# Performance work log

Hardware: AMD Instinct MI355X
Metric: run time of the kernel (lower is better)

Reference implementation:

```python
import jax, jax.numpy as jnp
import numpy as np

C = 512
C8 = C // 8  # query/key projection dim


def _conv1x1(x, W, b):
    # x: [B,C,H,W], W: [O,C], b: [O] -> [B,O,H,W]
    return jnp.einsum('bchw,oc->bohw', x, W) + b[None, :, None, None]


def setup_inputs() -> dict:
    key = jax.random.key(0)
    ks = jax.random.split(key, 13)
    B, H, Wd = 4, 64, 64
    s = 0.02
    return {
        'x_rgb': jax.random.normal(ks[0], (B, C, H, Wd), jnp.float32),
        'x_dep': jax.random.normal(ks[1], (B, C, H, Wd), jnp.float32),
        'Wq': jax.random.normal(ks[2], (C8, C), jnp.float32) * s,
        'bq': jnp.zeros((C8,), jnp.float32),
        'Wk': jax.random.normal(ks[3], (C8, C), jnp.float32) * s,
        'bk': jnp.zeros((C8,), jnp.float32),
        'Wdq': jax.random.normal(ks[4], (C8, C), jnp.float32) * s,
        'bdq': jnp.zeros((C8,), jnp.float32),
        'Wdk': jax.random.normal(ks[5], (C8, C), jnp.float32) * s,
        'bdk': jnp.zeros((C8,), jnp.float32),
        'Wv': jax.random.normal(ks[6], (C, C), jnp.float32) * s,
        'bv': jnp.zeros((C,), jnp.float32),
        'gamma': jnp.zeros((1,), jnp.float32),
    }


def reference(x_rgb, x_dep, Wq, bq, Wk, bk, Wdq, bdq, Wdk, bdk, Wv, bv, gamma):
    B, Cc, H, Wd = x_rgb.shape
    N = H * Wd
    # 1x1 conv projections, flattened over spatial positions -> [B, c, N]
    q = _conv1x1(x_rgb, Wq, bq).reshape(B, C8, N)
    k = _conv1x1(x_rgb, Wk, bk).reshape(B, C8, N)
    qd = _conv1x1(x_dep, Wdq, bdq).reshape(B, C8, N)
    kd = _conv1x1(x_dep, Wdk, bdk).reshape(B, C8, N)
    # fused dual-stream energy: [B, N, N]
    energy = jnp.einsum('bci,bcj->bij', q, k) + jnp.einsum('bci,bcj->bij', qd, kd)
    attention = jax.nn.softmax(energy, axis=-1)
    v = _conv1x1(x_rgb, Wv, bv).reshape(B, Cc, N)
    # out[b,c,i] = sum_j v[b,c,j] * attention[b,i,j]
    out = jnp.einsum('bcj,bij->bci', v, attention).reshape(B, Cc, H, Wd)
    return gamma[0] * out + x_rgb
```

## Files before the change

### kernel.cpp

```cpp
#include <hip/hip_runtime.h>
#include <math.h>

#define B_ 4
#define C_ 512
#define D_ 128
#define N_ 4096

typedef short s4v __attribute__((ext_vector_type(4)));
typedef short s8v __attribute__((ext_vector_type(8)));
typedef float f4v __attribute__((ext_vector_type(4)));

__device__ __forceinline__ unsigned short f2bf(float x) {
    union { float f; unsigned u; } v; v.f = x;
    unsigned r = v.u + 0x7FFF + ((v.u >> 16) & 1);
    return (unsigned short)(r >> 16);
}
__device__ __forceinline__ float bf2f(unsigned short h) {
    union { unsigned u; float f; } v; v.u = ((unsigned)h) << 16; return v.f;
}

__global__ __launch_bounds__(256) void cvt_w_kernel(
    const float* __restrict__ Wq,  const float* __restrict__ bq,
    const float* __restrict__ Wk,  const float* __restrict__ bk,
    const float* __restrict__ Wdq, const float* __restrict__ bdq,
    const float* __restrict__ Wdk, const float* __restrict__ bdk,
    const float* __restrict__ Wv,  const float* __restrict__ bv,
    unsigned short* __restrict__ Wb, float* __restrict__ biasb)
{
    int t = blockIdx.x * 256 + threadIdx.x;
    int e0 = t * 8;
    int row = e0 >> 9, c = e0 & 511;
    const float* src; int r0;
    if (row < 64)       { src = Wq;  r0 = row; }
    else if (row < 128) { src = Wk;  r0 = row - 64; }
    else if (row < 640) { src = Wv;  r0 = row - 128; }
    else if (row < 704) { src = Wdq; r0 = row - 640; }
    else                { src = Wdk; r0 = row - 704; }
    const float* p = src + (size_t)r0 * 512 + c;
    s8v o;
    #pragma unroll
    for (int u = 0; u < 8; ++u) ((unsigned short*)&o)[u] = f2bf(p[u]);
    *(s8v*)&Wb[e0] = o;
    if (blockIdx.x == 0) {
        #pragma unroll
        for (int s = 0; s < 3; ++s) {
            int o2 = threadIdx.x + 256 * s;
            float v;
            if (o2 < 64)       v = bq[o2];
            else if (o2 < 128) v = bk[o2 - 64];
            else if (o2 < 640) v = bv[o2 - 128];
            else if (o2 < 704) v = bdq[o2 - 640];
            else               v = bdk[o2 - 704];
            biasb[o2] = v;
        }
    }
}

__global__ __launch_bounds__(256) void xpose_kernel(
    const float* __restrict__ x_rgb, const float* __restrict__ x_dep,
    unsigned short* __restrict__ Xt)
{
    __shared__ __align__(16) unsigned short Ls[64 * 72];
    const int cT = blockIdx.x & 7, iT = blockIdx.x >> 3;
    const int b = blockIdx.y, st = blockIdx.z;
    const int t = threadIdx.x;
    const float* Xb = (st ? x_dep : x_rgb) + (size_t)b * C_ * N_;

    const int c4 = t >> 4, i4 = t & 15;
    {
        const float* xp = Xb + (size_t)(cT * 64 + c4 * 4) * N_ + iT * 64 + i4 * 4;
        float4 r0 = *(const float4*)(xp);
        float4 r1 = *(const float4*)(xp + N_);
        float4 r2 = *(const float4*)(xp + 2 * N_);
        float4 r3 = *(const float4*)(xp + 3 * N_);
        s4v p0 = { (short)f2bf(r0.x), (short)f2bf(r1.x), (short)f2bf(r2.x), (short)f2bf(r3.x) };
        s4v p1 = { (short)f2bf(r0.y), (short)f2bf(r1.y), (short)f2bf(r2.y), (short)f2bf(r3.y) };
        s4v p2 = { (short)f2bf(r0.z), (short)f2bf(r1.z), (short)f2bf(r2.z), (short)f2bf(r3.z) };
        s4v p3 = { (short)f2bf(r0.w), (short)f2bf(r1.w), (short)f2bf(r2.w), (short)f2bf(r3.w) };
        *(s4v*)&Ls[(i4 * 4 + 0) * 72 + c4 * 4] = p0;
        *(s4v*)&Ls[(i4 * 4 + 1) * 72 + c4 * 4] = p1;
        *(s4v*)&Ls[(i4 * 4 + 2) * 72 + c4 * 4] = p2;
        *(s4v*)&Ls[(i4 * 4 + 3) * 72 + c4 * 4] = p3;
    }
    __syncthreads();
    unsigned short* dst = Xt + ((size_t)(st * 4 + b) * N_ + iT * 64) * 512 + cT * 64;
    #pragma unroll
    for (int s = 0; s < 2; ++s) {
        int lin = t + 256 * s;
        int row = lin >> 3, g = lin & 7;
        *(s8v*)&dst[(size_t)row * 512 + g * 8] = *(const s8v*)&Ls[row * 72 + g * 8];
    }
}

__global__ __launch_bounds__(256) void gemm_kernel(
    const unsigned short* __restrict__ Wb, const float* __restrict__ biasb,
    const unsigned short* __restrict__ Xt,
    unsigned short* __restrict__ Q, unsigned short* __restrict__ K,
    unsigned short* __restrict__ V)
{
    __shared__ __align__(16) unsigned short Ws[128 * 64];
    __shared__ __align__(16) unsigned short Xs[128 * 64];
    const int b  = blockIdx.x >> 5;
    const int i0 = (blockIdx.x & 31) * 128;
    const int by = blockIdx.y;
    const int mbase = by * 128;
    const int st = (by == 5);
    const int t = threadIdx.x, w = t >> 6;
    const int lane = t & 63, col = lane & 15, quad = lane >> 4;
    const int mh = (w & 1) * 64, nh = (w >> 1) * 64;

    const unsigned short* Wg = Wb + (size_t)mbase * 512;
    const unsigned short* Xg = Xt + ((size_t)(st * 4 + b) * N_ + i0) * 512;

    f4v acc[4][4];
    #pragma unroll
    for (int mt = 0; mt < 4; ++mt)
        #pragma unroll
        for (int nt = 0; nt < 4; ++nt) acc[mt][nt] = (f4v){0.f, 0.f, 0.f, 0.f};

    for (int kc = 0; kc < 8; ++kc) {
        const int k0 = kc * 64;
        s8v wt[4], xt[4];
        #pragma unroll
        for (int s = 0; s < 4; ++s) {
            int lin = t + 256 * s;
            int row = lin >> 3, g = lin & 7;
            wt[s] = *(const s8v*)&Wg[(size_t)row * 512 + k0 + g * 8];
            xt[s] = *(const s8v*)&Xg[(size_t)row * 512 + k0 + g * 8];
        }
        __syncthreads();
        #pragma unroll
        for (int s = 0; s < 4; ++s) {
            int lin = t + 256 * s;
            int row = lin >> 3, g = lin & 7;
            int soff = row * 64 + ((g ^ (row & 7)) * 8);
            *(s8v*)&Ws[soff] = wt[s];
            *(s8v*)&Xs[soff] = xt[s];
        }
        __syncthreads();
        #pragma unroll
        for (int kk = 0; kk < 2; ++kk) {
            const int gq = kk * 4 + quad;
            s8v af[4], bf[4];
            #pragma unroll
            for (int mt = 0; mt < 4; ++mt) {
                int r = mh + mt * 16 + col;
                af[mt] = *(const s8v*)&Ws[r * 64 + ((gq ^ (r & 7)) * 8)];
            }
            #pragma unroll
            for (int nt = 0; nt < 4; ++nt) {
                int r = nh + nt * 16 + col;
                bf[nt] = *(const s8v*)&Xs[r * 64 + ((gq ^ (r & 7)) * 8)];
            }
            #pragma unroll
            for (int nt = 0; nt < 4; ++nt)
                #pragma unroll
                for (int mt = 0; mt < 4; ++mt)
                    acc[mt][nt] = __builtin_amdgcn_mfma_f32_16x16x32_bf16(
                        af[mt], bf[nt], acc[mt][nt], 0, 0, 0);
        }
    }

    const int mlo0 = mbase + mh;
    #pragma unroll
    for (int mt = 0; mt < 4; ++mt) {
        const int mlo = mlo0 + mt * 16;
        f4v bi = *(const f4v*)&biasb[mlo + quad * 4];
        if (mlo < 128 || mlo >= 640) {
            unsigned short* dst; int dbase;
            if (mlo < 64)       { dst = Q; dbase = mlo; }
            else if (mlo < 128) { dst = K; dbase = mlo - 64; }
            else if (mlo < 704) { dst = Q; dbase = 64 + (mlo - 640); }
            else                { dst = K; dbase = 64 + (mlo - 704); }
            #pragma unroll
            for (int nt = 0; nt < 4; ++nt) {
                int i = i0 + nh + nt * 16 + col;
                s4v pk = { (short)f2bf(acc[mt][nt][0] + bi[0]),
                           (short)f2bf(acc[mt][nt][1] + bi[1]),
                           (short)f2bf(acc[mt][nt][2] + bi[2]),
                           (short)f2bf(acc[mt][nt][3] + bi[3]) };
                *(s4v*)&dst[((size_t)b * N_ + i) * D_ + dbase + quad * 4] = pk;
            }
        } else {
            int c0 = mlo - 128 + quad * 4;
            #pragma unroll
            for (int nt = 0; nt < 4; ++nt) {
                int i = i0 + nh + nt * 16 + col;
                #pragma unroll
                for (int r = 0; r < 4; ++r)
                    V[((size_t)b * C_ + c0 + r) * N_ + i] =
                        f2bf(acc[mt][nt][r] + bi[r]);
            }
        }
    }
}

__global__ __launch_bounds__(256, 2) void attn_kernel(
    const unsigned short* __restrict__ Q, const unsigned short* __restrict__ K,
    const unsigned short* __restrict__ V,
    unsigned short* __restrict__ O_ws, float* __restrict__ l_ws)
{
    __shared__ __align__(16) unsigned short Ks[2][32 * 136];
    __shared__ __align__(16) unsigned short Ps[2][64 * 40];
    __shared__ float lred[2][64];

    const int id  = blockIdx.x;
    const int grp = id & 7;
    const int b   = grp & 3;
    const int jh  = grp >> 2;
    const int it  = id >> 3;
    const int i0  = it * 64;
    const int jb  = jh * 2048;
    const int t = threadIdx.x, w = t >> 6;
    const int lane = t & 63, col = lane & 15, quad = lane >> 4;
    const int ih = w & 1, jq = w >> 1;

    const unsigned short* Kg = K + (size_t)b * N_ * D_;
    const unsigned short* Vg = V + (size_t)b * C_ * N_;

    s8v qf[2][4];
    #pragma unroll
    for (int ig = 0; ig < 2; ++ig) {
        const unsigned short* qr =
            Q + ((size_t)b * N_ + i0 + ih * 32 + ig * 16 + col) * D_ + quad * 8;
        #pragma unroll
        for (int kk = 0; kk < 4; ++kk) qf[ig][kk] = *(const s8v*)(qr + kk * 32);
    }

    f4v accO[4][8];
    #pragma unroll
    for (int rt = 0; rt < 4; ++rt)
        #pragma unroll
        for (int ct = 0; ct < 8; ++ct) accO[rt][ct] = (f4v){0.f, 0.f, 0.f, 0.f};
    float lsum[2] = {0.f, 0.f};

    const unsigned short* Vt = Vg + (size_t)(w * 128 + col) * N_ + quad * 8;

    #pragma unroll
    for (int s = 0; s < 2; ++s) {
        int gi = t + 256 * s;
        s8v kv = *(const s8v*)&Kg[(size_t)(jb + (gi >> 4)) * D_ + (gi & 15) * 8];
        *(s8v*)&Ks[0][(gi >> 4) * 136 + (gi & 15) * 8] = kv;
    }
    asm volatile("s_waitcnt lgkmcnt(0)" ::: "memory");
    __builtin_amdgcn_s_barrier();

    for (int tt = 0; tt < 64; ++tt) {
        const int cur = tt & 1;
        const int j0 = jb + tt * 32;

        s8v kt[2];
        if (tt < 63) {
            #pragma unroll
            for (int s = 0; s < 2; ++s) {
                int gi = t + 256 * s;
                kt[s] = *(const s8v*)&Kg[(size_t)(j0 + 32 + (gi >> 4)) * D_ + (gi & 15) * 8];
            }
        }
        __builtin_amdgcn_sched_barrier(0);
        s8v vf[8];
        #pragma unroll
        for (int ct = 0; ct < 8; ++ct)
            vf[ct] = *(const s8v*)(Vt + (size_t)(ct * 16) * N_ + j0);

        f4v s0 = (f4v){0.f, 0.f, 0.f, 0.f};
        f4v s1 = (f4v){0.f, 0.f, 0.f, 0.f};
        #pragma unroll
        for (int kk = 0; kk < 4; ++kk) {
            s8v kf = *(const s8v*)&Ks[cur][(jq * 16 + col) * 136 + kk * 32 + quad * 8];
            s0 = __builtin_amdgcn_mfma_f32_16x16x32_bf16(kf, qf[0][kk], s0, 0, 0, 0);
            s1 = __builtin_amdgcn_mfma_f32_16x16x32_bf16(kf, qf[1][kk], s1, 0, 0, 0);
        }
        #pragma unroll
        for (int ig = 0; ig < 2; ++ig) {
            f4v sv = ig ? s1 : s0;
            s4v p; float ls = 0.f;
            #pragma unroll
            for (int r = 0; r < 4; ++r) {
                float e = __expf(sv[r]);
                ls += e;
                p[r] = (short)f2bf(e);
            }
            lsum[ig] += ls;
            *(s4v*)&Ps[cur][(ih * 32 + ig * 16 + col) * 40 + jq * 16 + quad * 4] = p;
        }
        if (tt < 63) {
            #pragma unroll
            for (int s = 0; s < 2; ++s) {
                int gi = t + 256 * s;
                *(s8v*)&Ks[cur ^ 1][(gi >> 4) * 136 + (gi & 15) * 8] = kt[s];
            }
        }
        asm volatile("s_waitcnt lgkmcnt(0)" ::: "memory");
        __builtin_amdgcn_s_barrier();

        s8v pf[4];
        #pragma unroll
        for (int rt = 0; rt < 4; ++rt)
            pf[rt] = *(const s8v*)&Ps[cur][(rt * 16 + col) * 40 + quad * 8];
        __builtin_amdgcn_s_setprio(1);
        #pragma unroll
        for (int ct = 0; ct < 8; ++ct)
            #pragma unroll
            for (int rt = 0; rt < 4; ++rt)
                accO[rt][ct] = __builtin_amdgcn_mfma_f32_16x16x32_bf16(
                    pf[rt], vf[ct], accO[rt][ct], 0, 0, 0);
        __builtin_amdgcn_s_setprio(0);
    }

    #pragma unroll
    for (int ig = 0; ig < 2; ++ig) {
        float v = lsum[ig];
        v += __shfl_xor(v, 16);
        v += __shfl_xor(v, 32);
        if (quad == 0) lred[jq][ih * 32 + ig * 16 + col] = v;
    }
    __syncthreads();
    if (t < 64)
        l_ws[((size_t)jh * B_ + b) * N_ + i0 + t] = lred[0][t] + lred[1][t];

    const size_t wbase =
        ((((size_t)jh * B_ + b) * 64 + it) * 4 + w) * 8192;
    #pragma unroll
    for (int ct = 0; ct < 8; ++ct)
        #pragma unroll
        for (int rt = 0; rt < 4; ++rt) {
            s4v pk = { (short)f2bf(accO[rt][ct][0]), (short)f2bf(accO[rt][ct][1]),
                       (short)f2bf(accO[rt][ct][2]), (short)f2bf(accO[rt][ct][3]) };
            *(s4v*)&O_ws[wbase + (size_t)(ct * 4 + rt) * 256 + lane * 4] = pk;
        }
}

__global__ __launch_bounds__(256) void combine_kernel(
    const unsigned short* __restrict__ O_ws, const float* __restrict__ l_ws,
    const float* __restrict__ x_rgb, const float* __restrict__ gamma,
    float* __restrict__ out)
{
    const size_t half = (size_t)B_ * 64 * 4 * 8192;
    int idx = blockIdx.x * 256 + threadIdx.x;
    int i4 = idx & 1023;
    int c  = (idx >> 10) & 511;
    int b  = idx >> 19;
    int i  = i4 * 4;
    int i0b = i >> 6, il = i & 63;
    int rt = il >> 4, qd = (il >> 2) & 3;
    int w = c >> 7, cl = c & 127, ct = cl >> 4, col = cl & 15;
    size_t obase = (((size_t)b * 64 + i0b) * 4 + w) * 8192
                 + (size_t)(ct * 4 + rt) * 256 + (qd * 16 + col) * 4;
    s4v o0 = *(const s4v*)&O_ws[obase];
    s4v o1 = *(const s4v*)&O_ws[half + obase];
    float4 l0 = *(const float4*)&l_ws[(size_t)b * N_ + i];
    float4 l1 = *(const float4*)&l_ws[(size_t)(B_ + b) * N_ + i];
    size_t base = ((size_t)b * C_ + c) * N_ + i;
    float4 x4 = *(const float4*)&x_rgb[base];
    float g = gamma[0];
    float4 r;
    r.x = g * (bf2f((unsigned short)o0[0]) + bf2f((unsigned short)o1[0])) / (l0.x + l1.x) + x4.x;
    r.y = g * (bf2f((unsigned short)o0[1]) + bf2f((unsigned short)o1[1])) / (l0.y + l1.y) + x4.y;
    r.z = g * (bf2f((unsigned short)o0[2]) + bf2f((unsigned short)o1[2])) / (l0.z + l1.z) + x4.z;
    r.w = g * (bf2f((unsigned short)o0[3]) + bf2f((unsigned short)o1[3])) / (l0.w + l1.w) + x4.w;
    *(float4*)&out[base] = r;
}

extern "C" void kernel_launch(void* const* d_in, const int* in_sizes, int n_in,
                              void* d_out, int out_size, void* d_ws, size_t ws_size,
                              hipStream_t stream) {
    (void)in_sizes; (void)n_in; (void)out_size; (void)ws_size;
    const float* x_rgb = (const float*)d_in[0];
    const float* x_dep = (const float*)d_in[1];
    const float* Wq    = (const float*)d_in[2];
    const float* bq    = (const float*)d_in[3];
    const float* Wk    = (const float*)d_in[4];
    const float* bk    = (const float*)d_in[5];
    const float* Wdq   = (const float*)d_in[6];
    const float* bdq   = (const float*)d_in[7];
    const float* Wdk   = (const float*)d_in[8];
    const float* bdk   = (const float*)d_in[9];
    const float* Wv    = (const float*)d_in[10];
    const float* bv    = (const float*)d_in[11];
    const float* gamma = (const float*)d_in[12];
    float* out = (float*)d_out;

    unsigned short* Q     = (unsigned short*)d_ws;
    unsigned short* K     = Q + (size_t)B_ * N_ * D_;
    unsigned short* V     = K + (size_t)B_ * N_ * D_;
    unsigned short* Wb    = V + (size_t)B_ * C_ * N_;
    float*          biasb = (float*)(Wb + 768 * 512);
    unsigned short* XtO   = (unsigned short*)(biasb + 1024);
    float*          l_ws  = (float*)(XtO + (size_t)2 * B_ * C_ * N_);

    cvt_w_kernel<<<dim3(192), 256, 0, stream>>>(
        Wq, bq, Wk, bk, Wdq, bdq, Wdk, bdk, Wv, bv, Wb, biasb);
    xpose_kernel<<<dim3(512, 4, 2), 256, 0, stream>>>(x_rgb, x_dep, XtO);
    gemm_kernel<<<dim3(128, 6), 256, 0, stream>>>(Wb, biasb, XtO, Q, K, V);
    attn_kernel<<<dim3(512), 256, 0, stream>>>(Q, K, V, XtO, l_ws);
    combine_kernel<<<dim3(8192), 256, 0, stream>>>(XtO, l_ws, x_rgb, gamma, out);
}
```

Measured before the change: 308.6 us.

## Stage V tiles through swizzled LDS with register prefetch instead of direct global loads

Each V tile (512 channels x 32 positions) is now loaded cooperatively with coalesced 16-byte reads into registers one iteration ahead, then written to a swizzled shared-memory buffer. The PV MFMA operands are read from LDS rather than through per-wave strided global loads. P is single-buffered and a second barrier per iteration is added, and the QK MFMAs get raised priority. The intent is to improve V load coalescing and hide its latency, at the cost of extra LDS traffic (32 KB more shared memory, which may reduce occupancy), more registers and an extra barrier.

```diff
diff --git a/kernel.cpp b/kernel.cpp
--- a/kernel.cpp
+++ b/kernel.cpp
@@ -201,7 +201,8 @@
     unsigned short* __restrict__ O_ws, float* __restrict__ l_ws)
 {
     __shared__ __align__(16) unsigned short Ks[2][32 * 136];
-    __shared__ __align__(16) unsigned short Ps[2][64 * 40];
+    __shared__ __align__(16) unsigned short Ps[64 * 40];
+    __shared__ __align__(16) unsigned short Vs[512 * 32];
     __shared__ float lred[2][64];
 
     const int id  = blockIdx.x;
@@ -234,8 +235,12 @@
         for (int ct = 0; ct < 8; ++ct) accO[rt][ct] = (f4v){0.f, 0.f, 0.f, 0.f};
     float lsum[2] = {0.f, 0.f};
 
-    const unsigned short* Vt = Vg + (size_t)(w * 128 + col) * N_ + quad * 8;
-
+    s8v vtp[8];
+    #pragma unroll
+    for (int s = 0; s < 8; ++s) {
+        int gi = t + 256 * s;
+        vtp[s] = *(const s8v*)&Vg[(size_t)(gi >> 2) * N_ + jb + (gi & 3) * 8];
+    }
     #pragma unroll
     for (int s = 0; s < 2; ++s) {
         int gi = t + 256 * s;
@@ -246,49 +251,58 @@
     __builtin_amdgcn_s_barrier();
 
     for (int tt = 0; tt < 64; ++tt) {
-        const int cur = tt & 1;
+        const int p = tt & 1;
         const int j0 = jb + tt * 32;
 
-        s8v kt[2];
+        s8v kt[2], vt[8];
         if (tt < 63) {
             #pragma unroll
             for (int s = 0; s < 2; ++s) {
                 int gi = t + 256 * s;
                 kt[s] = *(const s8v*)&Kg[(size_t)(j0 + 32 + (gi >> 4)) * D_ + (gi & 15) * 8];
             }
+            #pragma unroll
+            for (int s = 0; s < 8; ++s) {
+                int gi = t + 256 * s;
+                vt[s] = *(const s8v*)&Vg[(size_t)(gi >> 2) * N_ + j0 + 32 + (gi & 3) * 8];
+            }
         }
         __builtin_amdgcn_sched_barrier(0);
-        s8v vf[8];
-        #pragma unroll
-        for (int ct = 0; ct < 8; ++ct)
-            vf[ct] = *(const s8v*)(Vt + (size_t)(ct * 16) * N_ + j0);
-
+        #pragma unroll
+        for (int s = 0; s < 8; ++s) {
+            int gi = t + 256 * s;
+            int c = gi >> 2, g = gi & 3;
+            int sw = (g + c + (c >> 2)) & 3;
+            *(s8v*)&Vs[c * 32 + sw * 8] = vtp[s];
+        }
         f4v s0 = (f4v){0.f, 0.f, 0.f, 0.f};
         f4v s1 = (f4v){0.f, 0.f, 0.f, 0.f};
+        __builtin_amdgcn_s_setprio(1);
         #pragma unroll
         for (int kk = 0; kk < 4; ++kk) {
-            s8v kf = *(const s8v*)&Ks[cur][(jq * 16 + col) * 136 + kk * 32 + quad * 8];
+            s8v kf = *(const s8v*)&Ks[p][(jq * 16 + col) * 136 + kk * 32 + quad * 8];
             s0 = __builtin_amdgcn_mfma_f32_16x16x32_bf16(kf, qf[0][kk], s0, 0, 0, 0);
             s1 = __builtin_amdgcn_mfma_f32_16x16x32_bf16(kf, qf[1][kk], s1, 0, 0, 0);
         }
+        __builtin_amdgcn_s_setprio(0);
         #pragma unroll
         for (int ig = 0; ig < 2; ++ig) {
             f4v sv = ig ? s1 : s0;
-            s4v p; float ls = 0.f;
+            s4v pp; float ls = 0.f;
             #pragma unroll
             for (int r = 0; r < 4; ++r) {
                 float e = __expf(sv[r]);
                 ls += e;
-                p[r] = (short)f2bf(e);
+                pp[r] = (short)f2bf(e);
             }
             lsum[ig] += ls;
-            *(s4v*)&Ps[cur][(ih * 32 + ig * 16 + col) * 40 + jq * 16 + quad * 4] = p;
+            *(s4v*)&Ps[(ih * 32 + ig * 16 + col) * 40 + jq * 16 + quad * 4] = pp;
         }
         if (tt < 63) {
             #pragma unroll
             for (int s = 0; s < 2; ++s) {
                 int gi = t + 256 * s;
-                *(s8v*)&Ks[cur ^ 1][(gi >> 4) * 136 + (gi & 15) * 8] = kt[s];
+                *(s8v*)&Ks[p ^ 1][(gi >> 4) * 136 + (gi & 15) * 8] = kt[s];
             }
         }
         asm volatile("s_waitcnt lgkmcnt(0)" ::: "memory");
@@ -297,15 +311,26 @@
         s8v pf[4];
         #pragma unroll
         for (int rt = 0; rt < 4; ++rt)
-            pf[rt] = *(const s8v*)&Ps[cur][(rt * 16 + col) * 40 + quad * 8];
+            pf[rt] = *(const s8v*)&Ps[(rt * 16 + col) * 40 + quad * 8];
         __builtin_amdgcn_s_setprio(1);
         #pragma unroll
-        for (int ct = 0; ct < 8; ++ct)
+        for (int ct = 0; ct < 8; ++ct) {
+            int row = w * 128 + ct * 16 + col;
+            int sw = (quad + row + (row >> 2)) & 3;
+            s8v vfr = *(const s8v*)&Vs[row * 32 + sw * 8];
             #pragma unroll
             for (int rt = 0; rt < 4; ++rt)
                 accO[rt][ct] = __builtin_amdgcn_mfma_f32_16x16x32_bf16(
-                    pf[rt], vf[ct], accO[rt][ct], 0, 0, 0);
+                    pf[rt], vfr, accO[rt][ct], 0, 0, 0);
+        }
         __builtin_amdgcn_s_setprio(0);
+        asm volatile("s_waitcnt lgkmcnt(0)" ::: "memory");
+        __builtin_amdgcn_s_barrier();
+
+        if (tt < 63) {
+            #pragma unroll
+            for (int s = 0; s < 8; ++s) vtp[s] = vt[s];
+        }
     }
 
     #pragma unroll
```

After: 355.2 us. 1.15x slower.
